# Kernel optimization log

Hardware: AMD Instinct MI355X
Metric: run time of the kernel (lower is better)

The kernel has to match this reference:

```python
import jax, jax.numpy as jnp
import numpy as np

B, C, H, W = 2048, 512, 4, 4
T, D, NH, HD, FF, NL = 16, 512, 8, 64, 1024, 4
EPS = 1e-5
SCALE = float(1.0 / np.sqrt(HD))


def _make_adj(h, w):
    # torch_geometric.utils.grid(h, w): 3x3 neighborhood incl. self-loop;
    # GCNConv sym-normalizes: A_hat = D^-1/2 A D^-1/2
    n = h * w
    A = np.zeros((n, n), np.float32)
    for r in range(h):
        for c in range(w):
            for dr in (-1, 0, 1):
                for dc in (-1, 0, 1):
                    rr, cc = r + dr, c + dc
                    if 0 <= rr < h and 0 <= cc < w:
                        A[r * w + c, rr * w + cc] = 1.0
    dinv = 1.0 / np.sqrt(A.sum(1))
    return (A * dinv[:, None] * dinv[None, :]).astype(np.float32)


def setup_inputs():
    key = jax.random.key(0)
    ks = iter(jax.random.split(key, 64))
    def w(*s):
        return jax.random.normal(next(ks), s, jnp.float32) * 0.02
    return dict(
        x=jax.random.normal(next(ks), (B, C, H, W), jnp.float32),
        emb_w=w(D, D), emb_b=jnp.zeros((D,), jnp.float32),
        emb_ln_g=jnp.ones((D,), jnp.float32), emb_ln_b=jnp.zeros((D,), jnp.float32),
        pos=w(1, T, D),
        attn_wq=w(NL, D, D), attn_wk=w(NL, D, D), attn_wv=w(NL, D, D),
        attn_bq=jnp.zeros((NL, D), jnp.float32), attn_bk=jnp.zeros((NL, D), jnp.float32),
        attn_bv=jnp.zeros((NL, D), jnp.float32),
        attn_wo=w(NL, D, D), attn_bo=jnp.zeros((NL, D), jnp.float32),
        ln1_g=jnp.ones((NL, D), jnp.float32), ln1_b=jnp.zeros((NL, D), jnp.float32),
        ff_w1=w(NL, D, FF), ff_b1=jnp.zeros((NL, FF), jnp.float32),
        ff_w2=w(NL, FF, D), ff_b2=jnp.zeros((NL, D), jnp.float32),
        ln2_g=jnp.ones((NL, D), jnp.float32), ln2_b=jnp.zeros((NL, D), jnp.float32),
        fc_w=w(D, D), fc_b=jnp.zeros((D,), jnp.float32),
        fc_ln_g=jnp.ones((D,), jnp.float32), fc_ln_b=jnp.zeros((D,), jnp.float32),
        gcn_w1=w(C, 2 * C), gcn_b1=jnp.zeros((2 * C,), jnp.float32),
        gcn_ln1_g=jnp.ones((2 * C,), jnp.float32), gcn_ln1_b=jnp.zeros((2 * C,), jnp.float32),
        gcn_w2=w(2 * C, C), gcn_b2=jnp.zeros((C,), jnp.float32),
        gcn_ln2_g=jnp.ones((C,), jnp.float32), gcn_ln2_b=jnp.zeros((C,), jnp.float32),
        fusion_w=w(C, 2 * C), fusion_b=jnp.zeros((C,), jnp.float32),
        adj=jnp.asarray(_make_adj(H, W)),
    )


def _ln(x, g, b):
    mu = x.mean(-1, keepdims=True)
    var = ((x - mu) ** 2).mean(-1, keepdims=True)
    return (x - mu) * jax.lax.rsqrt(var + EPS) * g + b


def reference(x, emb_w, emb_b, emb_ln_g, emb_ln_b, pos,
              attn_wq, attn_wk, attn_wv, attn_bq, attn_bk, attn_bv, attn_wo, attn_bo,
              ln1_g, ln1_b, ff_w1, ff_b1, ff_w2, ff_b2, ln2_g, ln2_b,
              fc_w, fc_b, fc_ln_g, fc_ln_b,
              gcn_w1, gcn_b1, gcn_ln1_g, gcn_ln1_b, gcn_w2, gcn_b2, gcn_ln2_g, gcn_ln2_b,
              fusion_w, fusion_b, adj):
    Bx = x.shape[0]
    # ---- transformer branch: tokens = 16 spatial positions, dim 512 ----
    h = x.reshape(Bx, C, T).transpose(0, 2, 1)                 # [B,T,D]
    h = _ln(h @ emb_w + emb_b, emb_ln_g, emb_ln_b) + pos
    for i in range(NL):  # post-norm TransformerEncoderLayer, ReLU, eval (no dropout)
        q = (h @ attn_wq[i] + attn_bq[i]).reshape(Bx, T, NH, HD).transpose(0, 2, 1, 3)
        k = (h @ attn_wk[i] + attn_bk[i]).reshape(Bx, T, NH, HD).transpose(0, 2, 1, 3)
        v = (h @ attn_wv[i] + attn_bv[i]).reshape(Bx, T, NH, HD).transpose(0, 2, 1, 3)
        a = jax.nn.softmax(jnp.einsum('bhqd,bhkd->bhqk', q, k) * SCALE, axis=-1)
        o = jnp.einsum('bhqk,bhkd->bhqd', a, v).transpose(0, 2, 1, 3).reshape(Bx, T, D)
        h = _ln(h + o @ attn_wo[i] + attn_bo[i], ln1_g[i], ln1_b[i])
        f = jax.nn.relu(h @ ff_w1[i] + ff_b1[i]) @ ff_w2[i] + ff_b2[i]
        h = _ln(h + f, ln2_g[i], ln2_b[i])
    h = _ln(h @ fc_w + fc_b, fc_ln_g, fc_ln_b)
    x1 = h.transpose(0, 2, 1).reshape(Bx, C, H, W)
    # ---- GCN branch: dense normalized adjacency over the 16-node grid ----
    xn = x.transpose(0, 2, 3, 1).reshape(Bx, T, C)             # [B,16,C]
    g = jnp.einsum('mn,bnd->bmd', adj, xn @ gcn_w1) + gcn_b1   # GCNConv1 (bias after aggr)
    g = jax.nn.elu(_ln(g, gcn_ln1_g, gcn_ln1_b))
    g = jnp.einsum('mn,bnd->bmd', adj, g @ gcn_w2) + gcn_b2    # GCNConv2
    g = jax.nn.elu(_ln(g, gcn_ln2_g, gcn_ln2_b))
    x2 = g.reshape(Bx, H, W, C).transpose(0, 3, 1, 2)
    # ---- fusion: 1x1 conv + InstanceNorm2d (no affine) + ELU ----
    xc = jnp.concatenate([x1, x2], axis=1)                     # [B,2C,H,W]
    y = jnp.einsum('oc,bchw->bohw', fusion_w, xc) + fusion_b[None, :, None, None]
    mu = y.mean((2, 3), keepdims=True)
    var = ((y - mu) ** 2).mean((2, 3), keepdims=True)
    y = (y - mu) * jax.lax.rsqrt(var + EPS)
    return jax.nn.elu(y)
```

## Files before the change

kernel.cpp:

```cpp
#include <hip/hip_runtime.h>


typedef _Float16 f16;
typedef f16 f16x8 __attribute__((ext_vector_type(8)));
typedef f16 f16x4 __attribute__((ext_vector_type(4)));
typedef float f32x4 __attribute__((ext_vector_type(4)));

__device__ inline float wred_sum(float s) {
#pragma unroll
  for (int m = 32; m; m >>= 1) s += __shfl_xor(s, m);
  return s;
}

struct WDesc {
  const float* src;
  f16* dst;
  int K, N, tiles_n, tile_base, mode;
};
struct WTable {
  WDesc d[32];
  int n;
};

__global__ void wconvert_kernel(WTable tab) {
  const int tile = blockIdx.x;
  int di = 0;
  while (di + 1 < tab.n && tab.d[di + 1].tile_base <= tile) ++di;
  const WDesc w = tab.d[di];
  const int t = tile - w.tile_base;
  const int tk = t / w.tiles_n, tn = t % w.tiles_n;
  const int tid = threadIdx.x;
  const int rr = tid >> 5, cc = tid & 31;
  __shared__ float tb[32][33];
  if (w.mode == 0) {
#pragma unroll
    for (int i = 0; i < 4; i++) {
      const int k = tk * 32 + i * 8 + rr, n = tn * 32 + cc;
      tb[i * 8 + rr][cc] = w.src[(size_t)k * w.N + n];
    }
    __syncthreads();
#pragma unroll
    for (int i = 0; i < 4; i++) {
      const int n = tn * 32 + i * 8 + rr, k = tk * 32 + cc;
      w.dst[(size_t)n * w.K + k] = (f16)tb[cc][i * 8 + rr];
    }
  } else {
#pragma unroll
    for (int i = 0; i < 4; i++) {
      const int k = tk * 32 + i * 8 + rr, n = tn * 32 + cc;
      w.dst[(size_t)k * w.N + n] = (f16)w.src[(size_t)k * w.N + n];
    }
  }
}

__global__ void biaspack_kernel(const float* __restrict__ bq,
                                const float* __restrict__ bk,
                                const float* __restrict__ bv,
                                float* __restrict__ bqkv) {
  const int i = blockIdx.x * 256 + threadIdx.x;
  if (i >= 4 * 1536) return;
  const int l = i / 1536, j = i % 1536;
  float v;
  if (j < 512)       v = bq[l * 512 + j];
  else if (j < 1024) v = bk[l * 512 + j - 512];
  else               v = bv[l * 512 + j - 1024];
  bqkv[i] = v;
}

__global__ void prep_kernel(const float* __restrict__ x, f16* __restrict__ X0) {
  const int b = blockIdx.x;
  for (int c = threadIdx.x; c < 512; c += 256) {
    const float* src = x + ((size_t)b * 512 + c) * 16;
    float vals[16];
#pragma unroll
    for (int i = 0; i < 4; i++) {
      const float4 v = ((const float4*)src)[i];
      vals[i * 4 + 0] = v.x; vals[i * 4 + 1] = v.y;
      vals[i * 4 + 2] = v.z; vals[i * 4 + 3] = v.w;
    }
#pragma unroll
    for (int t = 0; t < 16; t++)
      X0[((size_t)b * 16 + t) * 512 + c] = (f16)vals[t];
  }
}

template <int OUT, bool RELU, bool HASB, int NT>
__global__ __launch_bounds__(512) void gemm256_kernel(
    const f16* __restrict__ A, const f16* __restrict__ Bt, void* __restrict__ C,
    const float* __restrict__ bias, const f16* __restrict__ resp,
    int N, int lda, int ldb) {
  __shared__ alignas(16) f16 sm[4][16384];
  const int tid = threadIdx.x;
  const int nb = N >> 8;
  const int cpx = gridDim.x >> 3;
  const int wg = (blockIdx.x & 7) * cpx + (blockIdx.x >> 3);
  const int bx = wg % nb, by = wg / nb;
  const int row0 = by << 8, col0 = bx << 8;
  const int lane = tid & 63;
  const int wid = tid >> 6;
  const int wm = (wid >> 2) << 7;
  const int wn = (wid & 3) << 6;
  const int srow = tid >> 2;
  const int schunk = (tid & 3) ^ ((tid >> 3) & 3);
  const f16* gA = A + (size_t)(row0 + srow) * lda + (schunk << 3);
  const f16* gB = Bt + (size_t)(col0 + srow) * ldb + (schunk << 3);
  const unsigned ldsw = (unsigned)(tid & 0x1C0) << 3;
  f32x4 acc[8][4] = {};
  const int rm = lane & 15;
  const int kg = lane >> 4;
  const int koff = (kg ^ ((rm >> 1) & 3)) << 3;

  auto STAGE = [&](int t) {
    f16* base = sm[t & 3];
    const int kt = t << 5;
    __builtin_amdgcn_global_load_lds(
        (const __attribute__((address_space(1))) void*)(gA + kt),
        (__attribute__((address_space(3))) void*)(base + ldsw), 16, 0, 0);
    __builtin_amdgcn_global_load_lds(
        (const __attribute__((address_space(1))) void*)(gA + (size_t)128 * lda + kt),
        (__attribute__((address_space(3))) void*)(base + 4096 + ldsw), 16, 0, 0);
    __builtin_amdgcn_global_load_lds(
        (const __attribute__((address_space(1))) void*)(gB + kt),
        (__attribute__((address_space(3))) void*)(base + 8192 + ldsw), 16, 0, 0);
    __builtin_amdgcn_global_load_lds(
        (const __attribute__((address_space(1))) void*)(gB + (size_t)128 * ldb + kt),
        (__attribute__((address_space(3))) void*)(base + 12288 + ldsw), 16, 0, 0);
  };

  STAGE(0);
  STAGE(1);
  STAGE(2);
  asm volatile("s_waitcnt vmcnt(8)" ::: "memory");
  __builtin_amdgcn_s_barrier();
  __builtin_amdgcn_sched_barrier(0);

#pragma unroll 1
  for (int t = 0; t < NT; ++t) {
    if (t + 3 < NT) STAGE(t + 3);
    const f16* As = sm[t & 3];
    const f16* Bs = As + 8192;
    f16x8 af[8], bf[4];
#pragma unroll
    for (int n = 0; n < 4; ++n)
      bf[n] = *(const f16x8*)(Bs + ((wn + n * 16 + rm) << 5) + koff);
#pragma unroll
    for (int m = 0; m < 8; ++m)
      af[m] = *(const f16x8*)(As + ((wm + m * 16 + rm) << 5) + koff);
    __builtin_amdgcn_s_setprio(1);
#pragma unroll
    for (int m = 0; m < 8; ++m)
#pragma unroll
      for (int n = 0; n < 4; ++n)
        acc[m][n] =
            __builtin_amdgcn_mfma_f32_16x16x32_f16(af[m], bf[n], acc[m][n], 0, 0, 0);
    __builtin_amdgcn_s_setprio(0);
    if (t + 3 < NT) {
      asm volatile("s_waitcnt vmcnt(8)" ::: "memory");
    } else if (t + 2 < NT) {
      asm volatile("s_waitcnt vmcnt(4)" ::: "memory");
    } else if (t + 1 < NT) {
      asm volatile("s_waitcnt vmcnt(0)" ::: "memory");
    }
    if (t + 1 < NT) {
      __builtin_amdgcn_s_barrier();
      __builtin_amdgcn_sched_barrier(0);
    }
  }

  const int cn = lane & 15;
  const int rg = (lane >> 4) << 2;
  if (OUT == 3) {
    float* out = (float*)C;
#pragma unroll
    for (int m = 0; m < 8; ++m) {
      const int bidx = (row0 >> 4) + (wm >> 4) + m;
#pragma unroll
      for (int n = 0; n < 4; ++n) {
        const int col = col0 + wn + n * 16 + cn;
        const float v0 = acc[m][n][0], v1 = acc[m][n][1];
        const float v2 = acc[m][n][2], v3 = acc[m][n][3];
        float s = v0 + v1 + v2 + v3;
        s += __shfl_xor(s, 16);
        s += __shfl_xor(s, 32);
        const float mu = s * (1.f / 16.f);
        float q = (v0 - mu) * (v0 - mu) + (v1 - mu) * (v1 - mu) +
                  (v2 - mu) * (v2 - mu) + (v3 - mu) * (v3 - mu);
        q += __shfl_xor(q, 16);
        q += __shfl_xor(q, 32);
        const float rstd = rsqrtf(q * (1.f / 16.f) + 1e-5f);
        float4 z;
        z.x = (v0 - mu) * rstd; z.x = z.x > 0.f ? z.x : expm1f(z.x);
        z.y = (v1 - mu) * rstd; z.y = z.y > 0.f ? z.y : expm1f(z.y);
        z.z = (v2 - mu) * rstd; z.z = z.z > 0.f ? z.z : expm1f(z.z);
        z.w = (v3 - mu) * rstd; z.w = z.w > 0.f ? z.w : expm1f(z.w);
        *(float4*)(out + ((size_t)bidx * 512 + col) * 16 + rg) = z;
      }
    }
  } else {
#pragma unroll
    for (int m = 0; m < 8; ++m) {
#pragma unroll
      for (int n = 0; n < 4; ++n) {
        const int col = col0 + wn + n * 16 + cn;
        const float bv = HASB ? bias[col] : 0.0f;
#pragma unroll
        for (int r = 0; r < 4; ++r) {
          const int row = row0 + wm + m * 16 + rg + r;
          float v = acc[m][n][r] + bv;
          if (OUT == 4) v += (float)resp[(size_t)row * N + col];
          if (RELU) v = v > 0.f ? v : 0.f;
          ((f16*)C)[(size_t)row * N + col] = (f16)v;
        }
      }
    }
  }
}

template <bool RES, bool POS>
__global__ void ln_kernel(const f16* in, const f16* res, const float* g,
                          const float* b, const float* pos, f16* out) {
  const int row = (blockIdx.x << 2) + (threadIdx.x >> 6);
  const int lane = threadIdx.x & 63;
  const int c0 = lane << 3;
  float v[8];
  const f16x8 xi = *(const f16x8*)(in + (size_t)row * 512 + c0);
  if (RES) {
    const f16x8 ri = *(const f16x8*)(res + (size_t)row * 512 + c0);
#pragma unroll
    for (int j = 0; j < 8; j++) v[j] = (float)xi[j] + (float)ri[j];
  } else {
#pragma unroll
    for (int j = 0; j < 8; j++) v[j] = (float)xi[j];
  }
  float s = 0;
#pragma unroll
  for (int j = 0; j < 8; j++) s += v[j];
  s = wred_sum(s);
  const float mu = s * (1.f / 512.f);
  float q = 0;
#pragma unroll
  for (int j = 0; j < 8; j++) {
    const float d = v[j] - mu;
    q += d * d;
  }
  q = wred_sum(q);
  const float rstd = rsqrtf(q * (1.f / 512.f) + 1e-5f);
  const int t = row & 15;
  f16x8 o8;
#pragma unroll
  for (int j = 0; j < 8; j++) {
    float o = (v[j] - mu) * rstd * g[c0 + j] + b[c0 + j];
    if (POS) o += pos[t * 512 + c0 + j];
    o8[j] = (f16)o;
  }
  *(f16x8*)(out + (size_t)row * 512 + c0) = o8;
}

__global__ void lnpack_kernel(const f16* __restrict__ in, const f16* __restrict__ x2,
                              const float* __restrict__ g, const float* __restrict__ b,
                              f16* __restrict__ F) {
  const int row = (blockIdx.x << 2) + (threadIdx.x >> 6);
  const int lane = threadIdx.x & 63;
  const int c0 = lane << 3;
  const f16x8 xi = *(const f16x8*)(in + (size_t)row * 512 + c0);
  float v[8];
#pragma unroll
  for (int j = 0; j < 8; j++) v[j] = (float)xi[j];
  float s = 0;
#pragma unroll
  for (int j = 0; j < 8; j++) s += v[j];
  s = wred_sum(s);
  const float mu = s * (1.f / 512.f);
  float q = 0;
#pragma unroll
  for (int j = 0; j < 8; j++) {
    const float d = v[j] - mu;
    q += d * d;
  }
  q = wred_sum(q);
  const float rstd = rsqrtf(q * (1.f / 512.f) + 1e-5f);
  f16x8 o8;
#pragma unroll
  for (int j = 0; j < 8; j++)
    o8[j] = (f16)((v[j] - mu) * rstd * g[c0 + j] + b[c0 + j]);
  *(f16x8*)(F + (size_t)row * 1024 + c0) = o8;
  const f16x8 x2v = *(const f16x8*)(x2 + (size_t)row * 512 + c0);
  *(f16x8*)(F + (size_t)row * 1024 + 512 + c0) = x2v;
}

__global__ __launch_bounds__(256) void attn_kernel(const f16* __restrict__ qkv,
                                                   f16* __restrict__ o) {
  __shared__ f16 smem[4][3776];
  const int wid = threadIdx.x >> 6;
  const int lane = threadIdx.x & 63;
  const int bh = (blockIdx.x << 2) + wid;
  const int b = bh >> 3, h = bh & 7;
  f16* W = smem[wid];
  f16* Qw = W;
  f16* Kw = W + 1152;
  f16* Vw = W + 2304;
  f16* Pw = W + 3456;
  const size_t base = (size_t)b * 24576 + (size_t)h * 64;
#pragma unroll
  for (int i = 0; i < 6; i++) {
    const int c = i * 64 + lane;
    const int t = c / 24;
    const int rem = c - t * 24;
    const int mat = rem >> 3, ch = rem & 7;
    const f16x8 v = *(const f16x8*)(qkv + base + (size_t)t * 1536 + mat * 512 + ch * 8);
    *(f16x8*)(W + mat * 1152 + t * 72 + ch * 8) = v;
  }
  __syncthreads();
  const int rm = lane & 15, kg = lane >> 4;
  f32x4 s4 = {};
  {
    const f16x8 q0 = *(const f16x8*)(Qw + rm * 72 + kg * 8);
    const f16x8 q1 = *(const f16x8*)(Qw + rm * 72 + 32 + kg * 8);
    const f16x8 k0 = *(const f16x8*)(Kw + rm * 72 + kg * 8);
    const f16x8 k1 = *(const f16x8*)(Kw + rm * 72 + 32 + kg * 8);
    s4 = __builtin_amdgcn_mfma_f32_16x16x32_f16(q0, k0, s4, 0, 0, 0);
    s4 = __builtin_amdgcn_mfma_f32_16x16x32_f16(q1, k1, s4, 0, 0, 0);
  }
  float p[4];
#pragma unroll
  for (int r = 0; r < 4; r++) {
    const float sv = s4[r] * 0.125f;
    float m = sv;
    m = fmaxf(m, __shfl_xor(m, 1));
    m = fmaxf(m, __shfl_xor(m, 2));
    m = fmaxf(m, __shfl_xor(m, 4));
    m = fmaxf(m, __shfl_xor(m, 8));
    const float e = expf(sv - m);
    float s = e;
    s += __shfl_xor(s, 1);
    s += __shfl_xor(s, 2);
    s += __shfl_xor(s, 4);
    s += __shfl_xor(s, 8);
    p[r] = e / s;
  }
#pragma unroll
  for (int r = 0; r < 4; r++) Pw[(kg * 4 + r) * 20 + rm] = (f16)p[r];
  __syncthreads();
  const f16x4 pa = *(const f16x4*)(Pw + rm * 20 + kg * 4);
  f32x4 o4[4] = {};
#pragma unroll
  for (int dt = 0; dt < 4; dt++) {
    f16x4 vb;
#pragma unroll
    for (int kk = 0; kk < 4; kk++) vb[kk] = Vw[(kg * 4 + kk) * 72 + dt * 16 + rm];
    o4[dt] = __builtin_amdgcn_mfma_f32_16x16x16f16(pa, vb, o4[dt], 0, 0, 0);
  }
  f16* op = o + (size_t)b * 16 * 512 + (size_t)h * 64;
#pragma unroll
  for (int dt = 0; dt < 4; dt++)
#pragma unroll
    for (int r = 0; r < 4; r++)
      op[(size_t)(kg * 4 + r) * 512 + dt * 16 + rm] = (f16)o4[dt][r];
}

template <int DG>
__global__ __launch_bounds__(256) void adjmix_kernel(
    const f16* __restrict__ r, const float* __restrict__ adj,
    const float* __restrict__ bias, const float* __restrict__ g,
    const float* __restrict__ bet, f16* __restrict__ out, int ldo) {
  const int b = blockIdx.x;
  const int tid = threadIdx.x;
  __shared__ float agg[16][DG];
  __shared__ float adjs[256];
  if (tid < 256) adjs[tid] = adj[tid];
  __syncthreads();
  const int d0 = tid * 4;
  if (d0 < DG) {
    float acc[16][4];
#pragma unroll
    for (int m = 0; m < 16; m++)
#pragma unroll
      for (int j = 0; j < 4; j++) acc[m][j] = 0.f;
#pragma unroll
    for (int n = 0; n < 16; n++) {
      const f16x4 v = *(const f16x4*)(r + ((size_t)b * 16 + n) * DG + d0);
      const float v0 = (float)v[0], v1 = (float)v[1], v2 = (float)v[2], v3 = (float)v[3];
#pragma unroll
      for (int m = 0; m < 16; m++) {
        const float a = adjs[m * 16 + n];
        acc[m][0] += a * v0;
        acc[m][1] += a * v1;
        acc[m][2] += a * v2;
        acc[m][3] += a * v3;
      }
    }
    const float4 bv = *(const float4*)(bias + d0);
#pragma unroll
    for (int m = 0; m < 16; m++) {
      agg[m][d0 + 0] = acc[m][0] + bv.x;
      agg[m][d0 + 1] = acc[m][1] + bv.y;
      agg[m][d0 + 2] = acc[m][2] + bv.z;
      agg[m][d0 + 3] = acc[m][3] + bv.w;
    }
  }
  __syncthreads();
  const int wave = tid >> 6, lane = tid & 63;
  for (int m = wave; m < 16; m += 4) {
    float s = 0;
#pragma unroll
    for (int j = 0; j < DG / 64; j++) s += agg[m][j * 64 + lane];
    s = wred_sum(s);
    const float mu = s / DG;
    float q = 0;
#pragma unroll
    for (int j = 0; j < DG / 64; j++) {
      const float t = agg[m][j * 64 + lane] - mu;
      q += t * t;
    }
    q = wred_sum(q);
    const float rstd = rsqrtf(q / DG + 1e-5f);
    const size_t grow = (size_t)b * 16 + m;
#pragma unroll
    for (int j = 0; j < DG / 64; j++) {
      const int d = j * 64 + lane;
      float v = (agg[m][d] - mu) * rstd * g[d] + bet[d];
      v = v > 0.f ? v : expm1f(v);
      out[grow * ldo + d] = (f16)v;
    }
  }
}

extern "C" void kernel_launch(void* const* d_in, const int* in_sizes, int n_in,
                              void* d_out, int out_size, void* d_ws, size_t ws_size,
                              hipStream_t stream) {
  (void)in_sizes; (void)n_in; (void)out_size; (void)ws_size;
  const float* x         = (const float*)d_in[0];
  const float* emb_w     = (const float*)d_in[1];
  const float* emb_b     = (const float*)d_in[2];
  const float* emb_ln_g  = (const float*)d_in[3];
  const float* emb_ln_b  = (const float*)d_in[4];
  const float* pos       = (const float*)d_in[5];
  const float* attn_wq   = (const float*)d_in[6];
  const float* attn_wk   = (const float*)d_in[7];
  const float* attn_wv   = (const float*)d_in[8];
  const float* attn_bq   = (const float*)d_in[9];
  const float* attn_bk   = (const float*)d_in[10];
  const float* attn_bv   = (const float*)d_in[11];
  const float* attn_wo   = (const float*)d_in[12];
  const float* attn_bo   = (const float*)d_in[13];
  const float* ln1_g     = (const float*)d_in[14];
  const float* ln1_b     = (const float*)d_in[15];
  const float* ff_w1     = (const float*)d_in[16];
  const float* ff_b1     = (const float*)d_in[17];
  const float* ff_w2     = (const float*)d_in[18];
  const float* ff_b2     = (const float*)d_in[19];
  const float* ln2_g     = (const float*)d_in[20];
  const float* ln2_b     = (const float*)d_in[21];
  const float* fc_w      = (const float*)d_in[22];
  const float* fc_b      = (const float*)d_in[23];
  const float* fc_ln_g   = (const float*)d_in[24];
  const float* fc_ln_b   = (const float*)d_in[25];
  const float* gcn_w1    = (const float*)d_in[26];
  const float* gcn_b1    = (const float*)d_in[27];
  const float* gcn_ln1_g = (const float*)d_in[28];
  const float* gcn_ln1_b = (const float*)d_in[29];
  const float* gcn_w2    = (const float*)d_in[30];
  const float* gcn_b2    = (const float*)d_in[31];
  const float* gcn_ln2_g = (const float*)d_in[32];
  const float* gcn_ln2_b = (const float*)d_in[33];
  const float* fusion_w  = (const float*)d_in[34];
  const float* fusion_b  = (const float*)d_in[35];
  const float* adj       = (const float*)d_in[36];
  (void)fusion_b;

  char* ws = (char*)d_ws;
  f16*   WF   = (f16*)(ws);
  float* BQKV = (float*)(ws + 20971520ull);
  f16*   Ap   = (f16*)(ws + 20996096ull);
  f16*   Bp   = (f16*)(ws + 54550528ull);
  f16*   Cp   = (f16*)(ws + 88104960ull);
  f16*   Qp   = (f16*)(ws + 121659392ull);

  const size_t o_emb = 0, o_qkv = 262144, o_wo = 3407872, o_ff1 = 4456448,
               o_ff2 = 6553600, o_fc = 8650752, o_g1 = 8912896, o_g2 = 9437184,
               o_fus = 9961472;

  WTable tab{};
  int ntab = 0, tbase = 0;
  auto add = [&](const float* s, f16* dst, int K, int N, int mode) {
    WDesc& w = tab.d[ntab++];
    w.src = s; w.dst = dst; w.K = K; w.N = N;
    w.tiles_n = N / 32; w.tile_base = tbase; w.mode = mode;
    tbase += (K / 32) * (N / 32);
  };
  add(emb_w, WF + o_emb, 512, 512, 0);
  for (int l = 0; l < 4; l++) {
    add(attn_wq + l * 262144, WF + o_qkv + (size_t)l * 786432, 512, 512, 0);
    add(attn_wk + l * 262144, WF + o_qkv + (size_t)l * 786432 + 262144, 512, 512, 0);
    add(attn_wv + l * 262144, WF + o_qkv + (size_t)l * 786432 + 524288, 512, 512, 0);
  }
  for (int l = 0; l < 4; l++)
    add(attn_wo + l * 262144, WF + o_wo + (size_t)l * 262144, 512, 512, 0);
  for (int l = 0; l < 4; l++)
    add(ff_w1 + l * 524288, WF + o_ff1 + (size_t)l * 524288, 512, 1024, 0);
  for (int l = 0; l < 4; l++)
    add(ff_w2 + l * 524288, WF + o_ff2 + (size_t)l * 524288, 1024, 512, 0);
  add(fc_w, WF + o_fc, 512, 512, 0);
  add(gcn_w1, WF + o_g1, 512, 1024, 0);
  add(gcn_w2, WF + o_g2, 1024, 512, 0);
  add(fusion_w, WF + o_fus, 512, 1024, 1);
  tab.n = ntab;

  wconvert_kernel<<<tbase, 256, 0, stream>>>(tab);
  biaspack_kernel<<<24, 256, 0, stream>>>(attn_bq, attn_bk, attn_bv, BQKV);
  prep_kernel<<<2048, 256, 0, stream>>>(x, Ap);

  gemm256_kernel<0, false, false, 16><<<512, 512, 0, stream>>>(
      Ap, WF + o_g1, Qp, nullptr, nullptr, 1024, 512, 512);
  adjmix_kernel<1024><<<2048, 256, 0, stream>>>(
      Qp, adj, gcn_b1, gcn_ln1_g, gcn_ln1_b, Bp, 1024);
  gemm256_kernel<0, false, false, 32><<<256, 512, 0, stream>>>(
      Bp, WF + o_g2, Qp, nullptr, nullptr, 512, 1024, 1024);

  gemm256_kernel<0, false, true, 16><<<256, 512, 0, stream>>>(
      Ap, WF + o_emb, Cp, emb_b, nullptr, 512, 512, 512);
  ln_kernel<false, true><<<8192, 256, 0, stream>>>(
      Cp, nullptr, emb_ln_g, emb_ln_b, pos, Bp);

  adjmix_kernel<512><<<2048, 256, 0, stream>>>(
      Qp, adj, gcn_b2, gcn_ln2_g, gcn_ln2_b, Ap, 512);

  for (int i = 0; i < 4; i++) {
    gemm256_kernel<0, false, true, 16><<<768, 512, 0, stream>>>(
        Bp, WF + o_qkv + (size_t)i * 786432, Qp, BQKV + i * 1536, nullptr,
        1536, 512, 512);
    attn_kernel<<<4096, 256, 0, stream>>>(Qp, Cp);
    gemm256_kernel<4, false, true, 16><<<256, 512, 0, stream>>>(
        Cp, WF + o_wo + (size_t)i * 262144, Qp, attn_bo + i * 512, Bp,
        512, 512, 512);
    ln_kernel<false, false><<<8192, 256, 0, stream>>>(
        Qp, nullptr, ln1_g + i * 512, ln1_b + i * 512, nullptr, Bp);
    gemm256_kernel<0, true, true, 16><<<512, 512, 0, stream>>>(
        Bp, WF + o_ff1 + (size_t)i * 524288, Qp, ff_b1 + i * 1024, nullptr,
        1024, 512, 512);
    gemm256_kernel<4, false, true, 32><<<256, 512, 0, stream>>>(
        Qp, WF + o_ff2 + (size_t)i * 524288, Qp + 33554432ull, ff_b2 + i * 512,
        Bp, 512, 1024, 1024);
    ln_kernel<false, false><<<8192, 256, 0, stream>>>(
        Qp + 33554432ull, nullptr, ln2_g + i * 512, ln2_b + i * 512, nullptr, Bp);
  }

  gemm256_kernel<0, false, true, 16><<<256, 512, 0, stream>>>(
      Bp, WF + o_fc, Qp, fc_b, nullptr, 512, 512, 512);
  lnpack_kernel<<<8192, 256, 0, stream>>>(Qp, Ap, fc_ln_g, fc_ln_b, Bp);

  gemm256_kernel<3, false, false, 32><<<256, 512, 0, stream>>>(
      Bp, WF + o_fus, d_out, nullptr, nullptr, 512, 1024, 1024);
}
```

Measured before the change: 1.310 ms.

## Restructure GEMM main loop into K=64 double-buffered tiles with interleaved phases

The GEMM K-tile grows from 32 to 64 and the ring goes from four buffers to two, each holding 32768 halves. Every tile is split into four phases, and each phase issues one slot of global-to-LDS loads for upcoming tiles alongside its MFMAs, with barriers at phase boundaries. The aim is to spread memory traffic evenly across compute and to reuse the B fragments over more MFMAs. The cost is many more barriers per tile, and the XOR swizzle changes to an 8-way pattern. NT template arguments are halved to match the larger K step.

```diff
diff --git a/kernel.cpp b/kernel.cpp
--- a/kernel.cpp
+++ b/kernel.cpp
@@ -84,12 +84,69 @@
   }
 }
 
+#define STAGE_SLOT(TI, ISB, HALF)                                              \
+  {                                                                            \
+    f16* dstb_ = smw + ((TI) & 1) * 32768 + ((ISB) ? 16384 : 0) +              \
+                 (HALF) * 8192 + ldsw2;                                        \
+    const int ld_ = (ISB) ? ldb : lda;                                         \
+    const f16* src_ = ((ISB) ? gBs : gAs) + (size_t)((HALF) * 128) * ld_ +     \
+                      ((size_t)(TI) << 6);                                     \
+    __builtin_amdgcn_global_load_lds(                                          \
+        (const __attribute__((address_space(1))) void*)(src_),                 \
+        (__attribute__((address_space(3))) void*)(dstb_), 16, 0, 0);           \
+    __builtin_amdgcn_global_load_lds(                                          \
+        (const __attribute__((address_space(1))) void*)(src_ + (size_t)64 * ld_), \
+        (__attribute__((address_space(3))) void*)(dstb_ + 4096), 16, 0, 0);    \
+  }
+
+#define VM4 asm volatile("s_waitcnt vmcnt(4)" ::: "memory");
+#define VM0 asm volatile("s_waitcnt vmcnt(0)" ::: "memory");
+#define VMN
+
+#define PHASE(TI, P, FIRST, DOSTG, STI, SISB, SHALF, VM)                       \
+  {                                                                            \
+    const f16* Ab_ = smw + ((TI) & 1) * 32768;                                 \
+    const f16* Bb_ = Ab_ + 16384;                                              \
+    if (FIRST) {                                                               \
+      _Pragma("unroll") for (int n = 0; n < 4; ++n) {                          \
+        const int r = wn + n * 16 + rm;                                        \
+        bf[n][0] = *(const f16x8*)(Bb_ + r * 64 + koff0);                      \
+        bf[n][1] = *(const f16x8*)(Bb_ + r * 64 + koff1);                      \
+      }                                                                        \
+    }                                                                          \
+    const int r0_ = wm + (2 * (P)) * 16 + rm;                                  \
+    const f16x8 a0k0 = *(const f16x8*)(Ab_ + r0_ * 64 + koff0);                \
+    const f16x8 a0k1 = *(const f16x8*)(Ab_ + r0_ * 64 + koff1);                \
+    const f16x8 a1k0 = *(const f16x8*)(Ab_ + (r0_ + 16) * 64 + koff0);         \
+    const f16x8 a1k1 = *(const f16x8*)(Ab_ + (r0_ + 16) * 64 + koff1);         \
+    if (DOSTG) STAGE_SLOT(STI, SISB, SHALF)                                    \
+    VM                                                                         \
+    __builtin_amdgcn_s_barrier();                                              \
+    asm volatile("s_waitcnt lgkmcnt(0)" ::: "memory");                         \
+    __builtin_amdgcn_sched_barrier(0);                                         \
+    __builtin_amdgcn_s_setprio(1);                                             \
+    _Pragma("unroll") for (int n = 0; n < 4; ++n) {                            \
+      acc[2 * (P)][n] = __builtin_amdgcn_mfma_f32_16x16x32_f16(                \
+          a0k0, bf[n][0], acc[2 * (P)][n], 0, 0, 0);                           \
+      acc[2 * (P)][n] = __builtin_amdgcn_mfma_f32_16x16x32_f16(                \
+          a0k1, bf[n][1], acc[2 * (P)][n], 0, 0, 0);                           \
+      acc[2 * (P) + 1][n] = __builtin_amdgcn_mfma_f32_16x16x32_f16(            \
+          a1k0, bf[n][0], acc[2 * (P) + 1][n], 0, 0, 0);                       \
+      acc[2 * (P) + 1][n] = __builtin_amdgcn_mfma_f32_16x16x32_f16(            \
+          a1k1, bf[n][1], acc[2 * (P) + 1][n], 0, 0, 0);                       \
+    }                                                                          \
+    __builtin_amdgcn_s_setprio(0);                                             \
+    __builtin_amdgcn_s_barrier();                                              \
+    __builtin_amdgcn_sched_barrier(0);                                         \
+  }
+
 template <int OUT, bool RELU, bool HASB, int NT>
 __global__ __launch_bounds__(512) void gemm256_kernel(
     const f16* __restrict__ A, const f16* __restrict__ Bt, void* __restrict__ C,
     const float* __restrict__ bias, const f16* __restrict__ resp,
     int N, int lda, int ldb) {
-  __shared__ alignas(16) f16 sm[4][16384];
+  __shared__ alignas(16) f16 smem[65536];
+  f16* smw = smem;
   const int tid = threadIdx.x;
   const int nb = N >> 8;
   const int cpx = gridDim.x >> 3;
@@ -100,71 +157,50 @@
   const int wid = tid >> 6;
   const int wm = (wid >> 2) << 7;
   const int wn = (wid & 3) << 6;
-  const int srow = tid >> 2;
-  const int schunk = (tid & 3) ^ ((tid >> 3) & 3);
-  const f16* gA = A + (size_t)(row0 + srow) * lda + (schunk << 3);
-  const f16* gB = Bt + (size_t)(col0 + srow) * ldb + (schunk << 3);
-  const unsigned ldsw = (unsigned)(tid & 0x1C0) << 3;
-  f32x4 acc[8][4] = {};
   const int rm = lane & 15;
   const int kg = lane >> 4;
-  const int koff = (kg ^ ((rm >> 1) & 3)) << 3;
-
-  auto STAGE = [&](int t) {
-    f16* base = sm[t & 3];
-    const int kt = t << 5;
-    __builtin_amdgcn_global_load_lds(
-        (const __attribute__((address_space(1))) void*)(gA + kt),
-        (__attribute__((address_space(3))) void*)(base + ldsw), 16, 0, 0);
-    __builtin_amdgcn_global_load_lds(
-        (const __attribute__((address_space(1))) void*)(gA + (size_t)128 * lda + kt),
-        (__attribute__((address_space(3))) void*)(base + 4096 + ldsw), 16, 0, 0);
-    __builtin_amdgcn_global_load_lds(
-        (const __attribute__((address_space(1))) void*)(gB + kt),
-        (__attribute__((address_space(3))) void*)(base + 8192 + ldsw), 16, 0, 0);
-    __builtin_amdgcn_global_load_lds(
-        (const __attribute__((address_space(1))) void*)(gB + (size_t)128 * ldb + kt),
-        (__attribute__((address_space(3))) void*)(base + 12288 + ldsw), 16, 0, 0);
-  };
-
-  STAGE(0);
-  STAGE(1);
-  STAGE(2);
-  asm volatile("s_waitcnt vmcnt(8)" ::: "memory");
+  const int key = rm & 7;
+  const int koff0 = ((kg ^ key)) << 3;
+  const int koff1 = (((4 + kg) ^ key)) << 3;
+  const int schunk = (tid & 7) ^ ((tid >> 3) & 7);
+  const f16* gAs = A + (size_t)(row0 + (tid >> 3)) * lda + (schunk << 3);
+  const f16* gBs = Bt + (size_t)(col0 + (tid >> 3)) * ldb + (schunk << 3);
+  const int ldsw2 = (tid & 0x1C0) << 3;
+  f32x4 acc[8][4] = {};
+  f16x8 bf[4][2];
+
+  STAGE_SLOT(0, 0, 0)
+  STAGE_SLOT(0, 0, 1)
+  STAGE_SLOT(0, 1, 0)
+  STAGE_SLOT(0, 1, 1)
+  STAGE_SLOT(1, 1, 0)
+  STAGE_SLOT(1, 1, 1)
+  VM4
   __builtin_amdgcn_s_barrier();
   __builtin_amdgcn_sched_barrier(0);
 
 #pragma unroll 1
-  for (int t = 0; t < NT; ++t) {
-    if (t + 3 < NT) STAGE(t + 3);
-    const f16* As = sm[t & 3];
-    const f16* Bs = As + 8192;
-    f16x8 af[8], bf[4];
-#pragma unroll
-    for (int n = 0; n < 4; ++n)
-      bf[n] = *(const f16x8*)(Bs + ((wn + n * 16 + rm) << 5) + koff);
-#pragma unroll
-    for (int m = 0; m < 8; ++m)
-      af[m] = *(const f16x8*)(As + ((wm + m * 16 + rm) << 5) + koff);
-    __builtin_amdgcn_s_setprio(1);
-#pragma unroll
-    for (int m = 0; m < 8; ++m)
-#pragma unroll
-      for (int n = 0; n < 4; ++n)
-        acc[m][n] =
-            __builtin_amdgcn_mfma_f32_16x16x32_f16(af[m], bf[n], acc[m][n], 0, 0, 0);
-    __builtin_amdgcn_s_setprio(0);
-    if (t + 3 < NT) {
-      asm volatile("s_waitcnt vmcnt(8)" ::: "memory");
-    } else if (t + 2 < NT) {
-      asm volatile("s_waitcnt vmcnt(4)" ::: "memory");
-    } else if (t + 1 < NT) {
-      asm volatile("s_waitcnt vmcnt(0)" ::: "memory");
-    }
-    if (t + 1 < NT) {
-      __builtin_amdgcn_s_barrier();
-      __builtin_amdgcn_sched_barrier(0);
-    }
+  for (int j = 0; j < NT / 2 - 1; ++j) {
+    const int u = 2 * j, v = u + 1, t2 = u + 2, t3 = u + 3;
+    PHASE(u, 0, true,  true, v,  0, 0, VMN)
+    PHASE(u, 1, false, true, v,  0, 1, VMN)
+    PHASE(u, 2, false, true, t2, 1, 0, VMN)
+    PHASE(u, 3, false, true, t2, 1, 1, VM4)
+    PHASE(v, 0, true,  true, t2, 0, 0, VMN)
+    PHASE(v, 1, false, true, t2, 0, 1, VMN)
+    PHASE(v, 2, false, true, t3, 1, 0, VMN)
+    PHASE(v, 3, false, true, t3, 1, 1, VM4)
+  }
+  {
+    const int u = NT - 2, v = NT - 1;
+    PHASE(u, 0, true,  true,  v, 0, 0, VMN)
+    PHASE(u, 1, false, true,  v, 0, 1, VMN)
+    PHASE(u, 2, false, false, 0, 0, 0, VMN)
+    PHASE(u, 3, false, false, 0, 0, 0, VM0)
+    PHASE(v, 0, true,  false, 0, 0, 0, VMN)
+    PHASE(v, 1, false, false, 0, 0, 0, VMN)
+    PHASE(v, 2, false, false, 0, 0, 0, VMN)
+    PHASE(v, 3, false, false, 0, 0, 0, VMN)
   }
 
   const int cn = lane & 15;
@@ -510,14 +546,14 @@
   biaspack_kernel<<<24, 256, 0, stream>>>(attn_bq, attn_bk, attn_bv, BQKV);
   prep_kernel<<<2048, 256, 0, stream>>>(x, Ap);
 
-  gemm256_kernel<0, false, false, 16><<<512, 512, 0, stream>>>(
+  gemm256_kernel<0, false, false, 8><<<512, 512, 0, stream>>>(
       Ap, WF + o_g1, Qp, nullptr, nullptr, 1024, 512, 512);
   adjmix_kernel<1024><<<2048, 256, 0, stream>>>(
       Qp, adj, gcn_b1, gcn_ln1_g, gcn_ln1_b, Bp, 1024);
-  gemm256_kernel<0, false, false, 32><<<256, 512, 0, stream>>>(
+  gemm256_kernel<0, false, false, 16><<<256, 512, 0, stream>>>(
       Bp, WF + o_g2, Qp, nullptr, nullptr, 512, 1024, 1024);
 
-  gemm256_kernel<0, false, true, 16><<<256, 512, 0, stream>>>(
+  gemm256_kernel<0, false, true, 8><<<256, 512, 0, stream>>>(
       Ap, WF + o_emb, Cp, emb_b, nullptr, 512, 512, 512);
   ln_kernel<false, true><<<8192, 256, 0, stream>>>(
       Cp, nullptr, emb_ln_g, emb_ln_b, pos, Bp);
@@ -526,29 +562,29 @@
       Qp, adj, gcn_b2, gcn_ln2_g, gcn_ln2_b, Ap, 512);
 
   for (int i = 0; i < 4; i++) {
-    gemm256_kernel<0, false, true, 16><<<768, 512, 0, stream>>>(
+    gemm256_kernel<0, false, true, 8><<<768, 512, 0, stream>>>(
         Bp, WF + o_qkv + (size_t)i * 786432, Qp, BQKV + i * 1536, nullptr,
         1536, 512, 512);
     attn_kernel<<<4096, 256, 0, stream>>>(Qp, Cp);
-    gemm256_kernel<4, false, true, 16><<<256, 512, 0, stream>>>(
+    gemm256_kernel<4, false, true, 8><<<256, 512, 0, stream>>>(
         Cp, WF + o_wo + (size_t)i * 262144, Qp, attn_bo + i * 512, Bp,
         512, 512, 512);
     ln_kernel<false, false><<<8192, 256, 0, stream>>>(
         Qp, nullptr, ln1_g + i * 512, ln1_b + i * 512, nullptr, Bp);
-    gemm256_kernel<0, true, true, 16><<<512, 512, 0, stream>>>(
+    gemm256_kernel<0, true, true, 8><<<512, 512, 0, stream>>>(
         Bp, WF + o_ff1 + (size_t)i * 524288, Qp, ff_b1 + i * 1024, nullptr,
         1024, 512, 512);
-    gemm256_kernel<4, false, true, 32><<<256, 512, 0, stream>>>(
+    gemm256_kernel<4, false, true, 16><<<256, 512, 0, stream>>>(
         Qp, WF + o_ff2 + (size_t)i * 524288, Qp + 33554432ull, ff_b2 + i * 512,
         Bp, 512, 1024, 1024);
     ln_kernel<false, false><<<8192, 256, 0, stream>>>(
         Qp + 33554432ull, nullptr, ln2_g + i * 512, ln2_b + i * 512, nullptr, Bp);
   }
 
-  gemm256_kernel<0, false, true, 16><<<256, 512, 0, stream>>>(
+  gemm256_kernel<0, false, true, 8><<<256, 512, 0, stream>>>(
       Bp, WF + o_fc, Qp, fc_b, nullptr, 512, 512, 512);
   lnpack_kernel<<<8192, 256, 0, stream>>>(Qp, Ap, fc_ln_g, fc_ln_b, Bp);
 
-  gemm256_kernel<3, false, false, 32><<<256, 512, 0, stream>>>(
+  gemm256_kernel<3, false, false, 16><<<256, 512, 0, stream>>>(
       Bp, WF + o_fus, d_out, nullptr, nullptr, 512, 1024, 1024);
 }
```

Result: no change. 1.291 ms, median of 3 (-1.5%).

## Shrink GEMM tile to 256x128 with 3-stage LDS pipeline and double the grids

Applied to the files above, without the earlier changes.

The GEMM kernel drops from 256x256 output tiles to 256x128, with 8 waves each owning a 64x64 sub-tile. The LDS pipeline goes from 4 stages to 3, so shared memory falls from 128KB to 72KB. Launch bounds now request 4 waves per SIMD and every grid size is doubled. The intent is more resident blocks per CU and better load balance across 256 CUs, at the cost of less data reuse per tile and a shallower prefetch pipeline.

```diff
diff --git a/kernel.cpp b/kernel.cpp
--- a/kernel.cpp
+++ b/kernel.cpp
@@ -85,83 +85,77 @@
 }
 
 template <int OUT, bool RELU, bool HASB, int NT>
-__global__ __launch_bounds__(512) void gemm256_kernel(
+__global__ __launch_bounds__(512, 4) void gemm256_kernel(
     const f16* __restrict__ A, const f16* __restrict__ Bt, void* __restrict__ C,
     const float* __restrict__ bias, const f16* __restrict__ resp,
     int N, int lda, int ldb) {
-  __shared__ alignas(16) f16 sm[4][16384];
+  __shared__ alignas(16) f16 sm[36864];
   const int tid = threadIdx.x;
-  const int nb = N >> 8;
+  const int nb = N >> 7;
   const int cpx = gridDim.x >> 3;
   const int wg = (blockIdx.x & 7) * cpx + (blockIdx.x >> 3);
   const int bx = wg % nb, by = wg / nb;
-  const int row0 = by << 8, col0 = bx << 8;
+  const int row0 = by << 8, col0 = bx << 7;
   const int lane = tid & 63;
   const int wid = tid >> 6;
-  const int wm = (wid >> 2) << 7;
-  const int wn = (wid & 3) << 6;
-  const int srow = tid >> 2;
-  const int schunk = (tid & 3) ^ ((tid >> 3) & 3);
-  const f16* gA = A + (size_t)(row0 + srow) * lda + (schunk << 3);
-  const f16* gB = Bt + (size_t)(col0 + srow) * ldb + (schunk << 3);
-  const unsigned ldsw = (unsigned)(tid & 0x1C0) << 3;
-  f32x4 acc[8][4] = {};
+  const int wm = (wid >> 1) << 6;
+  const int wn = (wid & 1) << 6;
   const int rm = lane & 15;
   const int kg = lane >> 4;
   const int koff = (kg ^ ((rm >> 1) & 3)) << 3;
+  const int srow = tid >> 2;
+  const int schunk = (tid & 3) ^ ((tid >> 3) & 3);
+  const f16* gAs = A + (size_t)(row0 + srow) * lda + (schunk << 3);
+  const f16* gBs = Bt + (size_t)(col0 + srow) * ldb + (schunk << 3);
+  const int ldsw = (tid & 0x1C0) << 3;
+  f32x4 acc[4][4] = {};
 
   auto STAGE = [&](int t) {
-    f16* base = sm[t & 3];
+    f16* buf = sm + (t % 3) * 12288;
     const int kt = t << 5;
     __builtin_amdgcn_global_load_lds(
-        (const __attribute__((address_space(1))) void*)(gA + kt),
-        (__attribute__((address_space(3))) void*)(base + ldsw), 16, 0, 0);
+        (const __attribute__((address_space(1))) void*)(gAs + kt),
+        (__attribute__((address_space(3))) void*)(buf + ldsw), 16, 0, 0);
     __builtin_amdgcn_global_load_lds(
-        (const __attribute__((address_space(1))) void*)(gA + (size_t)128 * lda + kt),
-        (__attribute__((address_space(3))) void*)(base + 4096 + ldsw), 16, 0, 0);
+        (const __attribute__((address_space(1))) void*)(gAs + (size_t)128 * lda + kt),
+        (__attribute__((address_space(3))) void*)(buf + 4096 + ldsw), 16, 0, 0);
     __builtin_amdgcn_global_load_lds(
-        (const __attribute__((address_space(1))) void*)(gB + kt),
-        (__attribute__((address_space(3))) void*)(base + 8192 + ldsw), 16, 0, 0);
-    __builtin_amdgcn_global_load_lds(
-        (const __attribute__((address_space(1))) void*)(gB + (size_t)128 * ldb + kt),
-        (__attribute__((address_space(3))) void*)(base + 12288 + ldsw), 16, 0, 0);
+        (const __attribute__((address_space(1))) void*)(gBs + kt),
+        (__attribute__((address_space(3))) void*)(buf + 8192 + ldsw), 16, 0, 0);
   };
 
   STAGE(0);
   STAGE(1);
-  STAGE(2);
-  asm volatile("s_waitcnt vmcnt(8)" ::: "memory");
+  asm volatile("s_waitcnt vmcnt(3)" ::: "memory");
   __builtin_amdgcn_s_barrier();
   __builtin_amdgcn_sched_barrier(0);
 
 #pragma unroll 1
   for (int t = 0; t < NT; ++t) {
-    if (t + 3 < NT) STAGE(t + 3);
-    const f16* As = sm[t & 3];
-    const f16* Bs = As + 8192;
-    f16x8 af[8], bf[4];
+    if (t + 2 < NT) STAGE(t + 2);
+    const f16* Ab = sm + (t % 3) * 12288;
+    const f16* Bb = Ab + 8192;
+    f16x8 af[4], bf[4];
 #pragma unroll
     for (int n = 0; n < 4; ++n)
-      bf[n] = *(const f16x8*)(Bs + ((wn + n * 16 + rm) << 5) + koff);
-#pragma unroll
-    for (int m = 0; m < 8; ++m)
-      af[m] = *(const f16x8*)(As + ((wm + m * 16 + rm) << 5) + koff);
+      bf[n] = *(const f16x8*)(Bb + ((wn + n * 16 + rm) << 5) + koff);
+#pragma unroll
+    for (int m = 0; m < 4; ++m)
+      af[m] = *(const f16x8*)(Ab + ((wm + m * 16 + rm) << 5) + koff);
     __builtin_amdgcn_s_setprio(1);
 #pragma unroll
-    for (int m = 0; m < 8; ++m)
+    for (int m = 0; m < 4; ++m)
 #pragma unroll
       for (int n = 0; n < 4; ++n)
         acc[m][n] =
             __builtin_amdgcn_mfma_f32_16x16x32_f16(af[m], bf[n], acc[m][n], 0, 0, 0);
     __builtin_amdgcn_s_setprio(0);
-    if (t + 3 < NT) {
-      asm volatile("s_waitcnt vmcnt(8)" ::: "memory");
-    } else if (t + 2 < NT) {
-      asm volatile("s_waitcnt vmcnt(4)" ::: "memory");
-    } else if (t + 1 < NT) {
-      asm volatile("s_waitcnt vmcnt(0)" ::: "memory");
-    }
     if (t + 1 < NT) {
+      if (t + 2 < NT) {
+        asm volatile("s_waitcnt vmcnt(3)" ::: "memory");
+      } else {
+        asm volatile("s_waitcnt vmcnt(0)" ::: "memory");
+      }
       __builtin_amdgcn_s_barrier();
       __builtin_amdgcn_sched_barrier(0);
     }
@@ -172,7 +166,7 @@
   if (OUT == 3) {
     float* out = (float*)C;
 #pragma unroll
-    for (int m = 0; m < 8; ++m) {
+    for (int m = 0; m < 4; ++m) {
       const int bidx = (row0 >> 4) + (wm >> 4) + m;
 #pragma unroll
       for (int n = 0; n < 4; ++n) {
@@ -198,7 +192,7 @@
     }
   } else {
 #pragma unroll
-    for (int m = 0; m < 8; ++m) {
+    for (int m = 0; m < 4; ++m) {
 #pragma unroll
       for (int n = 0; n < 4; ++n) {
         const int col = col0 + wn + n * 16 + cn;
@@ -510,14 +504,14 @@
   biaspack_kernel<<<24, 256, 0, stream>>>(attn_bq, attn_bk, attn_bv, BQKV);
   prep_kernel<<<2048, 256, 0, stream>>>(x, Ap);
 
-  gemm256_kernel<0, false, false, 16><<<512, 512, 0, stream>>>(
+  gemm256_kernel<0, false, false, 16><<<1024, 512, 0, stream>>>(
       Ap, WF + o_g1, Qp, nullptr, nullptr, 1024, 512, 512);
   adjmix_kernel<1024><<<2048, 256, 0, stream>>>(
       Qp, adj, gcn_b1, gcn_ln1_g, gcn_ln1_b, Bp, 1024);
-  gemm256_kernel<0, false, false, 32><<<256, 512, 0, stream>>>(
+  gemm256_kernel<0, false, false, 32><<<512, 512, 0, stream>>>(
       Bp, WF + o_g2, Qp, nullptr, nullptr, 512, 1024, 1024);
 
-  gemm256_kernel<0, false, true, 16><<<256, 512, 0, stream>>>(
+  gemm256_kernel<0, false, true, 16><<<512, 512, 0, stream>>>(
       Ap, WF + o_emb, Cp, emb_b, nullptr, 512, 512, 512);
   ln_kernel<false, true><<<8192, 256, 0, stream>>>(
       Cp, nullptr, emb_ln_g, emb_ln_b, pos, Bp);
@@ -526,29 +520,29 @@
       Qp, adj, gcn_b2, gcn_ln2_g, gcn_ln2_b, Ap, 512);
 
   for (int i = 0; i < 4; i++) {
-    gemm256_kernel<0, false, true, 16><<<768, 512, 0, stream>>>(
+    gemm256_kernel<0, false, true, 16><<<1536, 512, 0, stream>>>(
         Bp, WF + o_qkv + (size_t)i * 786432, Qp, BQKV + i * 1536, nullptr,
         1536, 512, 512);
     attn_kernel<<<4096, 256, 0, stream>>>(Qp, Cp);
-    gemm256_kernel<4, false, true, 16><<<256, 512, 0, stream>>>(
+    gemm256_kernel<4, false, true, 16><<<512, 512, 0, stream>>>(
         Cp, WF + o_wo + (size_t)i * 262144, Qp, attn_bo + i * 512, Bp,
         512, 512, 512);
     ln_kernel<false, false><<<8192, 256, 0, stream>>>(
         Qp, nullptr, ln1_g + i * 512, ln1_b + i * 512, nullptr, Bp);
-    gemm256_kernel<0, true, true, 16><<<512, 512, 0, stream>>>(
+    gemm256_kernel<0, true, true, 16><<<1024, 512, 0, stream>>>(
         Bp, WF + o_ff1 + (size_t)i * 524288, Qp, ff_b1 + i * 1024, nullptr,
         1024, 512, 512);
-    gemm256_kernel<4, false, true, 32><<<256, 512, 0, stream>>>(
+    gemm256_kernel<4, false, true, 32><<<512, 512, 0, stream>>>(
         Qp, WF + o_ff2 + (size_t)i * 524288, Qp + 33554432ull, ff_b2 + i * 512,
         Bp, 512, 1024, 1024);
     ln_kernel<false, false><<<8192, 256, 0, stream>>>(
         Qp + 33554432ull, nullptr, ln2_g + i * 512, ln2_b + i * 512, nullptr, Bp);
   }
 
-  gemm256_kernel<0, false, true, 16><<<256, 512, 0, stream>>>(
+  gemm256_kernel<0, false, true, 16><<<512, 512, 0, stream>>>(
       Bp, WF + o_fc, Qp, fc_b, nullptr, 512, 512, 512);
   lnpack_kernel<<<8192, 256, 0, stream>>>(Qp, Ap, fc_ln_g, fc_ln_b, Bp);
 
-  gemm256_kernel<3, false, false, 32><<<256, 512, 0, stream>>>(
+  gemm256_kernel<3, false, false, 32><<<512, 512, 0, stream>>>(
       Bp, WF + o_fus, d_out, nullptr, nullptr, 512, 1024, 1024);
 }
```

Measured after the change: 1.296 ms. No clear change (-1.1%).
